# Performance work log

Measured on AMD Instinct MI355X. Metric: run time of the kernel, lower is better.

## Reference

```python
import jax, jax.numpy as jnp
import numpy as np

N, E, D, ETYPES = 20000, 200000, 256, 16

def _gelu(x):
    return jax.nn.gelu(x, approximate=False)

def setup_inputs() -> dict:
    key = jax.random.key(0)
    ks = jax.random.split(key, 24)
    s = lambda k, shape, fan: (jax.random.normal(k, shape, jnp.float32) / np.sqrt(fan)).astype(jnp.float32)
    inp = {}
    inp['node_embeddings'] = jax.random.normal(ks[0], (N, D), jnp.float32)
    inp['edge_index'] = jax.random.randint(ks[1], (2, E), 0, N, jnp.int64 if jax.config.jax_enable_x64 else jnp.int32)
    inp['edge_type'] = jax.random.randint(ks[2], (E,), 0, ETYPES, jnp.int32)
    inp['task_embedding'] = jax.random.normal(ks[3], (D,), jnp.float32)
    inp['edge_emb'] = s(ks[4], (ETYPES, D), D)
    inp['msg_W'] = s(ks[5], (D, D), D); inp['msg_b'] = jnp.zeros((D,), jnp.float32)
    inp['att_W1'] = s(ks[6], (4 * D, D), 4 * D); inp['att_b1'] = jnp.zeros((D,), jnp.float32)
    inp['att_W2'] = s(ks[7], (D, 1), D); inp['att_b2'] = jnp.zeros((1,), jnp.float32)
    inp['edge_scale'] = jnp.asarray(0.5, jnp.float32)
    inp['ma_W1'] = s(ks[8], (D, 2 * D), D); inp['ma_b1'] = jnp.zeros((2 * D,), jnp.float32)
    inp['ma_W2'] = s(ks[9], (2 * D, 2 * D), 2 * D); inp['ma_b2'] = jnp.zeros((2 * D,), jnp.float32)
    inp['up_W1'] = s(ks[10], (2 * D, D), 2 * D); inp['up_b1'] = jnp.zeros((D,), jnp.float32)
    inp['up_W2'] = s(ks[11], (D, D), D); inp['up_b2'] = jnp.zeros((D,), jnp.float32)
    inp['ua_W1'] = s(ks[12], (D, 2 * D), D); inp['ua_b1'] = jnp.zeros((2 * D,), jnp.float32)
    inp['ua_W2'] = s(ks[13], (2 * D, 2 * D), 2 * D); inp['ua_b2'] = jnp.zeros((2 * D,), jnp.float32)
    inp['ln_g'] = jnp.ones((D,), jnp.float32); inp['ln_b'] = jnp.zeros((D,), jnp.float32)
    return inp

def reference(node_embeddings, edge_index, edge_type, task_embedding, edge_emb,
              msg_W, msg_b, att_W1, att_b1, att_W2, att_b2, edge_scale,
              ma_W1, ma_b1, ma_W2, ma_b2, up_W1, up_b1, up_W2, up_b2,
              ua_W1, ua_b1, ua_W2, ua_b2, ln_g, ln_b):
    n_nodes = node_embeddings.shape[0]
    src, dst = edge_index[0], edge_index[1]
    e = edge_emb[edge_type]                       # [E, D]
    x_src = node_embeddings[src]                  # [E, D]
    x_dst = node_embeddings[dst]                  # [E, D]
    messages = (x_src + e) @ msg_W + msg_b        # [E, D]
    # edge attention over [x_src, x_dst, edge_repr, task]
    task_rep = jnp.broadcast_to(task_embedding, (src.shape[0], task_embedding.shape[0]))
    att_in = jnp.concatenate([x_src, x_dst, e, task_rep], axis=-1)  # [E, 4D]
    edge_delta = jnp.tanh(_gelu(att_in @ att_W1 + att_b1) @ att_W2 + att_b2)  # [E, 1]
    edge_weight = 1.0 + edge_scale * edge_delta   # [E, 1]
    # FiLM-style message adapter from task embedding
    ma = _gelu(task_embedding @ ma_W1 + ma_b1) @ ma_W2 + ma_b2      # [2D]
    msg_gamma, msg_beta = ma[:ma.shape[0] // 2], ma[ma.shape[0] // 2:]
    messages = messages * (1.0 + 0.5 * jnp.tanh(msg_gamma)) + msg_beta
    messages = messages * edge_weight
    # scatter-add aggregation with degree normalization
    agg = jax.ops.segment_sum(messages, dst, num_segments=n_nodes)            # [N, D]
    deg = jax.ops.segment_sum(edge_weight[:, 0], dst, num_segments=n_nodes)   # [N]
    agg = agg / jnp.maximum(deg, 1.0)[:, None]
    ua = _gelu(task_embedding @ ua_W1 + ua_b1) @ ua_W2 + ua_b2      # [2D]
    upd_gamma, upd_beta = ua[:ua.shape[0] // 2], ua[ua.shape[0] // 2:]
    agg = agg * (1.0 + 0.5 * jnp.tanh(upd_gamma)) + upd_beta
    upd_in = jnp.concatenate([node_embeddings, agg], axis=-1)       # [N, 2D]
    updated = _gelu(upd_in @ up_W1 + up_b1) @ up_W2 + up_b2         # [N, D]
    y = node_embeddings + updated
    mu = jnp.mean(y, axis=-1, keepdims=True)
    var = jnp.mean((y - mu) ** 2, axis=-1, keepdims=True)
    return (y - mu) / jnp.sqrt(var + 1e-5) * ln_g + ln_b
```

## Files before the change

kernel.cpp:

```cpp
#include <hip/hip_runtime.h>
#include <hip/hip_bf16.h>

#define NN 20000
#define NE 200000

typedef __bf16 bf16x8 __attribute__((ext_vector_type(8)));
typedef float f32x4 __attribute__((ext_vector_type(4)));
typedef unsigned short u16x8 __attribute__((ext_vector_type(8)));

constexpr int TAB_MSG_SCALE = 0;
constexpr int TAB_MSG_BETA  = 256;
constexpr int TAB_UPD_SCALE = 512;
constexpr int TAB_UPD_BETA  = 768;
constexpr int TAB_TASKC     = 1024;
constexpr int TAB_ECM       = 1280;
constexpr size_t OFF_WPRET = 40960;
constexpr size_t OFF_W1T   = 434176;
constexpr size_t OFF_W2T   = 696320;
constexpr size_t OFF_CNT   = 827392;
constexpr size_t OFF_SRCET = 907392;
constexpr size_t OFF_UPDB  = 11147392;
constexpr size_t OFF_G     = 21387392;
constexpr size_t OFF_P2B   = 41867392;
constexpr size_t WS_NEED   = 52107392;

constexpr int ROW_BLOCKS = (NN + 63)/64;
constexpr int GEMM_GRID  = ROW_BLOCKS*4;
constexpr int CSR_BLOCKS = (NE + 255)/256;

__device__ __forceinline__ float bf2f(unsigned short u){
  union { unsigned int i; float f; } v; v.i = ((unsigned int)u) << 16; return v.f;
}
__device__ __forceinline__ unsigned short f2bf(float f){
  __bf16 h = (__bf16)f; unsigned short u; __builtin_memcpy(&u, &h, 2); return u;
}
__device__ __forceinline__ float gelu_f(float x){
  return 0.5f * x * (1.0f + erff(x * 0.70710678118654752f));
}
__device__ __forceinline__ float gelu_fast(float x){
  return x / (1.0f + __expf(-1.702f * x));
}
__device__ __forceinline__ float tanh_fast(float x){
  float e = __expf(2.0f * x);
  return 1.0f - 2.0f / (e + 1.0f);
}
__device__ __forceinline__ float sum16(const float* p){
  float a = ((p[0]+p[1])+(p[2]+p[3])) + ((p[4]+p[5])+(p[6]+p[7]));
  float b = ((p[8]+p[9])+(p[10]+p[11])) + ((p[12]+p[13])+(p[14]+p[15]));
  return a + b;
}

__global__ __launch_bounds__(256) void k_setup(
    const float* __restrict__ task, const float* __restrict__ eemb,
    const float* __restrict__ msg_W, const float* __restrict__ msg_b,
    const float* __restrict__ att_W1, const float* __restrict__ att_b1,
    const float* __restrict__ ma_W1, const float* __restrict__ ma_b1,
    const float* __restrict__ ma_W2, const float* __restrict__ ma_b2,
    const float* __restrict__ ua_W1, const float* __restrict__ ua_b1,
    const float* __restrict__ ua_W2, const float* __restrict__ ua_b2,
    const float* __restrict__ up_W1, const float* __restrict__ up_W2,
    float* __restrict__ tabs,
    unsigned short* __restrict__ WpreT, unsigned short* __restrict__ W1T,
    unsigned short* __restrict__ W2T)
{
  __shared__ float s_in[512];
  __shared__ float s_h[512];
  int bb = blockIdx.x, tid = threadIdx.x;
  if (bb >= 35){
    int b = bb - 35;
    if (b < 768){
      int n = b;
      float v;
      if (n < 256)      v = msg_W[tid*256 + n];
      else if (n < 512) v = att_W1[tid*256 + (n - 256)];
      else              v = att_W1[(256 + tid)*256 + (n - 512)];
      WpreT[n*256 + tid] = f2bf(v);
    } else if (b < 1024){
      int n = b - 768;
      W1T[n*512 + tid]       = f2bf(up_W1[tid*256 + n]);
      W1T[n*512 + 256 + tid] = f2bf(up_W1[(256 + tid)*256 + n]);
    } else {
      int n = b - 1024;
      W2T[n*256 + tid] = f2bf(up_W2[tid*256 + n]);
    }
    return;
  }
  int b = bb;
  if (b < 2){
    const float* W1 = b ? ua_W1 : ma_W1;  const float* b1 = b ? ua_b1 : ma_b1;
    const float* W2 = b ? ua_W2 : ma_W2;  const float* b2 = b ? ua_b2 : ma_b2;
    s_in[tid] = task[tid];
    __syncthreads();
    #pragma unroll
    for (int jj = 0; jj < 2; ++jj){
      int j = tid + jj*256;
      float pacc[16];
      #pragma unroll
      for (int u = 0; u < 16; ++u) pacc[u] = 0.f;
      for (int k0 = 0; k0 < 256; k0 += 16){
        float wv[16];
        #pragma unroll
        for (int u = 0; u < 16; ++u) wv[u] = W1[(k0 + u)*512 + j];
        #pragma unroll
        for (int u = 0; u < 16; ++u) pacc[u] += s_in[k0 + u] * wv[u];
      }
      s_h[j] = gelu_f(b1[j] + sum16(pacc));
    }
    __syncthreads();
    float o[2];
    #pragma unroll
    for (int jj = 0; jj < 2; ++jj){
      int j = tid + jj*256;
      float pacc[16];
      #pragma unroll
      for (int u = 0; u < 16; ++u) pacc[u] = 0.f;
      for (int k0 = 0; k0 < 512; k0 += 16){
        float wv[16];
        #pragma unroll
        for (int u = 0; u < 16; ++u) wv[u] = W2[(k0 + u)*512 + j];
        #pragma unroll
        for (int u = 0; u < 16; ++u) pacc[u] += s_h[k0 + u] * wv[u];
      }
      o[jj] = b2[j] + sum16(pacc);
    }
    float* scale = tabs + (b ? TAB_UPD_SCALE : TAB_MSG_SCALE);
    float* beta  = tabs + (b ? TAB_UPD_BETA  : TAB_MSG_BETA);
    scale[tid] = 1.0f + 0.5f * tanhf(o[0]);
    beta[tid]  = o[1];
  } else if (b == 2){
    s_in[tid] = task[tid];
    __syncthreads();
    float pacc[16];
    #pragma unroll
    for (int u = 0; u < 16; ++u) pacc[u] = 0.f;
    for (int k0 = 0; k0 < 256; k0 += 16){
      float wv[16];
      #pragma unroll
      for (int u = 0; u < 16; ++u) wv[u] = att_W1[(768 + k0 + u)*256 + tid];
      #pragma unroll
      for (int u = 0; u < 16; ++u) pacc[u] += s_in[k0 + u] * wv[u];
    }
    tabs[TAB_TASKC + tid] = att_b1[tid] + sum16(pacc);
  } else if (b < 19){
    int t = b - 3;
    s_in[tid] = eemb[t*256 + tid];
    __syncthreads();
    float pacc[16];
    #pragma unroll
    for (int u = 0; u < 16; ++u) pacc[u] = 0.f;
    for (int k0 = 0; k0 < 256; k0 += 16){
      float wv[16];
      #pragma unroll
      for (int u = 0; u < 16; ++u) wv[u] = msg_W[(k0 + u)*256 + tid];
      #pragma unroll
      for (int u = 0; u < 16; ++u) pacc[u] += s_in[k0 + u] * wv[u];
    }
    tabs[TAB_ECM + t*512 + ((tid >> 2) << 3) + 4 + (tid & 3)] = msg_b[tid] + sum16(pacc);
  } else {
    int t = b - 19;
    s_in[tid] = eemb[t*256 + tid];
    __syncthreads();
    float pacc[16];
    #pragma unroll
    for (int u = 0; u < 16; ++u) pacc[u] = 0.f;
    for (int k0 = 0; k0 < 256; k0 += 16){
      float wv[16];
      #pragma unroll
      for (int u = 0; u < 16; ++u) wv[u] = att_W1[(512 + k0 + u)*256 + tid];
      #pragma unroll
      for (int u = 0; u < 16; ++u) pacc[u] += s_in[k0 + u] * wv[u];
    }
    tabs[TAB_ECM + t*512 + ((tid >> 2) << 3) + (tid & 3)] = sum16(pacc);
  }
}

__global__ __launch_bounds__(256) void k_gemm_pre(
    const float* __restrict__ X, const unsigned short* __restrict__ WpreT,
    const float* __restrict__ tabs,
    const int* __restrict__ eidx, const int* __restrict__ etype,
    unsigned short* __restrict__ G, unsigned short* __restrict__ P2b,
    int* __restrict__ cnt, unsigned int* __restrict__ srcet)
{
  __shared__ __align__(16) unsigned short s_b[16*256];
  int tid = threadIdx.x;
  int bb = blockIdx.x;
  if (bb >= GEMM_GRID){
    int e = (bb - GEMM_GRID)*256 + tid;
    if (e < NE){
      int dst = eidx[NE + e];
      int pos = atomicAdd(&cnt[dst], 1);
      srcet[((unsigned)dst << 7) + pos] =
          (unsigned int)eidx[e] | ((unsigned int)etype[e] << 16);
    }
    return;
  }
  int rb = bb >> 2, chunk = bb & 3;
  int wv = tid >> 6, lane = tid & 63;
  int m0 = rb*64 + wv*16;
  bool valid = (m0 < NN);
  int lo = lane & 15, hi = lane >> 4;
  bf16x8 a[8];
  if (valid){
    const float* xrow = X + (size_t)(m0 + lo)*256 + hi*8;
    #pragma unroll
    for (int kc = 0; kc < 8; ++kc){
      float4 f0 = *(const float4*)(xrow + kc*32);
      float4 f1 = *(const float4*)(xrow + kc*32 + 4);
      bf16x8 v;
      v[0]=(__bf16)f0.x; v[1]=(__bf16)f0.y; v[2]=(__bf16)f0.z; v[3]=(__bf16)f0.w;
      v[4]=(__bf16)f1.x; v[5]=(__bf16)f1.y; v[6]=(__bf16)f1.z; v[7]=(__bf16)f1.w;
      a[kc] = v;
    }
  }
  int sn = tid >> 4, sk0 = (tid & 15)*16;
  int sswz = (sn & 7) << 3;
  int rswz = (lo & 7) << 3;
  for (int t = 0; t < 12; ++t){
    int nt = chunk*12 + t;
    __syncthreads();
    {
      const unsigned short* gsrc = WpreT + (size_t)(nt*16 + sn)*256 + sk0;
      uint4 d0 = *(const uint4*)(gsrc);
      uint4 d1 = *(const uint4*)(gsrc + 8);
      *(uint4*)(s_b + sn*256 + (sk0 ^ sswz))       = d0;
      *(uint4*)(s_b + sn*256 + ((sk0 + 8) ^ sswz)) = d1;
    }
    __syncthreads();
    if (!valid) continue;
    f32x4 acc = {0.f, 0.f, 0.f, 0.f};
    #pragma unroll
    for (int kc = 0; kc < 8; ++kc){
      bf16x8 bfrag = *(const bf16x8*)(s_b + lo*256 + ((kc*32 + hi*8) ^ rswz));
      acc = __builtin_amdgcn_mfma_f32_16x16x32_bf16(a[kc], bfrag, acc, 0, 0, 0);
    }
    int n0 = nt*16;
    if (nt < 16){
      int j = n0 + lo;
      unsigned short* grow = G + (size_t)(m0 + hi*4)*512 + 256 + j;
      #pragma unroll
      for (int r = 0; r < 4; ++r) grow[(size_t)r*512] = f2bf(acc[r]);
    } else if (nt < 32){
      int j = n0 - 256 + lo;
      unsigned short* grow = G + (size_t)(m0 + hi*4)*512 + j;
      #pragma unroll
      for (int r = 0; r < 4; ++r) grow[(size_t)r*512] = f2bf(acc[r]);
    } else {
      int j = n0 - 512 + lo;
      float tcadd = tabs[TAB_TASKC + j];
      unsigned short* prow = P2b + (size_t)(m0 + hi*4)*256 + j;
      #pragma unroll
      for (int r = 0; r < 4; ++r) prow[(size_t)r*256] = f2bf(acc[r] + tcadd);
    }
  }
}

__global__ __launch_bounds__(256) void k_agg(
    const int* __restrict__ cnt, const unsigned int* __restrict__ srcet,
    const unsigned short* __restrict__ G, const unsigned short* __restrict__ P2b,
    const float* __restrict__ tabs, const float* __restrict__ attW2,
    const float* __restrict__ attb2, const float* __restrict__ escale,
    unsigned short* __restrict__ updB)
{
  int wv = threadIdx.x >> 6, lane = threadIdx.x & 63;
  int h = lane >> 5, l = lane & 31;
  int node = blockIdx.x*8 + wv*2 + h;
  int d0 = l*8;
  float sc = escale[0], bb = attb2[0];

  float q[8], w2v[8];
  {
    u16x8 p2 = *(const u16x8*)(P2b + (size_t)node*256 + d0);
    #pragma unroll
    for (int j = 0; j < 8; ++j) q[j] = bf2f(p2[j]);
    float4 wa = *(const float4*)(attW2 + d0);
    float4 wb = *(const float4*)(attW2 + d0 + 4);
    w2v[0]=wa.x; w2v[1]=wa.y; w2v[2]=wa.z; w2v[3]=wa.w;
    w2v[4]=wb.x; w2v[5]=wb.y; w2v[6]=wb.z; w2v[7]=wb.w;
  }
  const float* ecm_base = tabs + TAB_ECM + (l << 4);

  int start = node << 7;
  int end = start + cnt[node];
  float acc[8];
  #pragma unroll
  for (int j = 0; j < 8; ++j) acc[j] = 0.f;
  float W = 0.f;

  unsigned int se0 = 0, se1 = 0;
  u16x8 p1a = {0,0,0,0,0,0,0,0}, mma = {0,0,0,0,0,0,0,0};
  if (start < end){
    se0 = srcet[start];
    const unsigned short* gr = G + (((unsigned)(se0 & 0xFFFFu)) << 9);
    p1a = *(const u16x8*)(gr + d0);
    mma = *(const u16x8*)(gr + 256 + d0);
    if (start + 1 < end) se1 = srcet[start + 1];
  }
  for (int i = start; i < end; ++i){
    u16x8 p1b = p1a, mmb = mma;
    unsigned int se2 = 0;
    if (i + 1 < end){
      const unsigned short* gr = G + (((unsigned)(se1 & 0xFFFFu)) << 9);
      p1b = *(const u16x8*)(gr + d0);
      mmb = *(const u16x8*)(gr + 256 + d0);
    }
    if (i + 2 < end) se2 = srcet[i + 2];
    int et = (int)(se0 >> 16);
    const float* ecm = ecm_base + (et << 9);
    float4 ec0 = *(const float4*)(ecm);
    float4 em0 = *(const float4*)(ecm + 4);
    float4 ec1 = *(const float4*)(ecm + 8);
    float4 em1 = *(const float4*)(ecm + 12);
    float part =
        gelu_fast(bf2f(p1a[0]) + q[0] + ec0.x)*w2v[0]
      + gelu_fast(bf2f(p1a[1]) + q[1] + ec0.y)*w2v[1]
      + gelu_fast(bf2f(p1a[2]) + q[2] + ec0.z)*w2v[2]
      + gelu_fast(bf2f(p1a[3]) + q[3] + ec0.w)*w2v[3]
      + gelu_fast(bf2f(p1a[4]) + q[4] + ec1.x)*w2v[4]
      + gelu_fast(bf2f(p1a[5]) + q[5] + ec1.y)*w2v[5]
      + gelu_fast(bf2f(p1a[6]) + q[6] + ec1.z)*w2v[6]
      + gelu_fast(bf2f(p1a[7]) + q[7] + ec1.w)*w2v[7];
    part += __shfl_xor(part, 1);
    part += __shfl_xor(part, 2);
    part += __shfl_xor(part, 4);
    part += __shfl_xor(part, 8);
    part += __shfl_xor(part, 16);
    float w = 1.0f + sc*tanh_fast(part + bb);
    acc[0] += w*(bf2f(mma[0]) + em0.x);
    acc[1] += w*(bf2f(mma[1]) + em0.y);
    acc[2] += w*(bf2f(mma[2]) + em0.z);
    acc[3] += w*(bf2f(mma[3]) + em0.w);
    acc[4] += w*(bf2f(mma[4]) + em1.x);
    acc[5] += w*(bf2f(mma[5]) + em1.y);
    acc[6] += w*(bf2f(mma[6]) + em1.z);
    acc[7] += w*(bf2f(mma[7]) + em1.w);
    W += w;
    se0 = se1; se1 = se2; p1a = p1b; mma = mmb;
  }

  float d = fmaxf(W, 1.0f), rd = 1.0f / d;
  unsigned short st[8];
  #pragma unroll
  for (int c = 0; c < 2; ++c){
    float4 ms = *(const float4*)(tabs + TAB_MSG_SCALE + d0 + c*4);
    float4 mb = *(const float4*)(tabs + TAB_MSG_BETA  + d0 + c*4);
    float4 us = *(const float4*)(tabs + TAB_UPD_SCALE + d0 + c*4);
    float4 ub = *(const float4*)(tabs + TAB_UPD_BETA  + d0 + c*4);
    st[c*4+0] = f2bf((ms.x*acc[c*4+0] + mb.x*W)*rd*us.x + ub.x);
    st[c*4+1] = f2bf((ms.y*acc[c*4+1] + mb.y*W)*rd*us.y + ub.y);
    st[c*4+2] = f2bf((ms.z*acc[c*4+2] + mb.z*W)*rd*us.z + ub.z);
    st[c*4+3] = f2bf((ms.w*acc[c*4+3] + mb.w*W)*rd*us.w + ub.w);
  }
  *(u16x8*)(updB + (size_t)node*256 + d0) = *(u16x8*)(st);
}

__device__ __forceinline__ bf16x8 ldA(const float* xrow, const unsigned short* urow, int ke){
  if (ke < 256){
    float4 f0 = *(const float4*)(xrow + ke);
    float4 f1 = *(const float4*)(xrow + ke + 4);
    bf16x8 v;
    v[0]=(__bf16)f0.x; v[1]=(__bf16)f0.y; v[2]=(__bf16)f0.z; v[3]=(__bf16)f0.w;
    v[4]=(__bf16)f1.x; v[5]=(__bf16)f1.y; v[6]=(__bf16)f1.z; v[7]=(__bf16)f1.w;
    return v;
  }
  return *(const bf16x8*)(urow + (ke - 256));
}

__global__ __launch_bounds__(256) void k_mlp(
    const float* __restrict__ X, const unsigned short* __restrict__ updB,
    const unsigned short* __restrict__ W1T, const unsigned short* __restrict__ W2T,
    const float* __restrict__ up_b1, const float* __restrict__ up_b2,
    const float* __restrict__ ln_g, const float* __restrict__ ln_b,
    float* __restrict__ out)
{
  __shared__ __align__(16) unsigned short s_H[32*256];
  __shared__ float s_sum[4*32], s_sq[4*32];
  __shared__ float s_mu[32], s_rs[32];
  int m0 = blockIdx.x*32;
  int tid = threadIdx.x;
  int wv = tid >> 6, lane = tid & 63, lo = lane & 15, hi = lane >> 4;

  const float* x0 = X + (size_t)(m0 + lo)*256;
  const float* x1 = x0 + 16*256;
  const unsigned short* u0 = updB + (size_t)(m0 + lo)*256;
  const unsigned short* u1 = u0 + 16*256;

  f32x4 acc0[4], acc1[4];
  #pragma unroll
  for (int t = 0; t < 4; ++t){
    float b = up_b1[wv*64 + t*16 + lo];
    acc0[t] = (f32x4){b, b, b, b};
    acc1[t] = acc0[t];
  }
  #pragma unroll
  for (int kc = 0; kc < 16; ++kc){
    int ke = kc*32 + hi*8;
    bf16x8 a0 = ldA(x0, u0, ke);
    bf16x8 a1 = ldA(x1, u1, ke);
    #pragma unroll
    for (int t = 0; t < 4; ++t){
      int n = wv*64 + t*16 + lo;
      bf16x8 bf = *(const bf16x8*)(W1T + (size_t)n*512 + ke);
      acc0[t] = __builtin_amdgcn_mfma_f32_16x16x32_bf16(a0, bf, acc0[t], 0, 0, 0);
      acc1[t] = __builtin_amdgcn_mfma_f32_16x16x32_bf16(a1, bf, acc1[t], 0, 0, 0);
    }
  }
  #pragma unroll
  for (int t = 0; t < 4; ++t){
    #pragma unroll
    for (int r = 0; r < 4; ++r){
      int row0 = hi*4 + r, n = wv*64 + t*16 + lo;
      s_H[(row0 << 8) | (n ^ ((row0 & 7) << 3))] = f2bf(gelu_fast(acc0[t][r]));
      int row1 = row0 + 16;
      s_H[(row1 << 8) | (n ^ ((row1 & 7) << 3))] = f2bf(gelu_fast(acc1[t][r]));
    }
  }
  __syncthreads();

  f32x4 y0[4], y1[4];
  #pragma unroll
  for (int t = 0; t < 4; ++t){
    float b = up_b2[wv*64 + t*16 + lo];
    y0[t] = (f32x4){b, b, b, b};
    y1[t] = y0[t];
  }
  #pragma unroll
  for (int kc = 0; kc < 8; ++kc){
    int ke = kc*32 + hi*8;
    bf16x8 af0 = *(const bf16x8*)(s_H + ((lo << 8) | (ke ^ ((lo & 7) << 3))));
    int r1 = lo + 16;
    bf16x8 af1 = *(const bf16x8*)(s_H + ((r1 << 8) | (ke ^ ((r1 & 7) << 3))));
    #pragma unroll
    for (int t = 0; t < 4; ++t){
      int n = wv*64 + t*16 + lo;
      bf16x8 bf = *(const bf16x8*)(W2T + (size_t)n*256 + ke);
      y0[t] = __builtin_amdgcn_mfma_f32_16x16x32_bf16(af0, bf, y0[t], 0, 0, 0);
      y1[t] = __builtin_amdgcn_mfma_f32_16x16x32_bf16(af1, bf, y1[t], 0, 0, 0);
    }
  }

  #pragma unroll
  for (int t = 0; t < 4; ++t){
    #pragma unroll
    for (int r = 0; r < 4; ++r){
      int row0 = hi*4 + r, n = wv*64 + t*16 + lo;
      y0[t][r] += X[(size_t)(m0 + row0)*256 + n];
      y1[t][r] += X[(size_t)(m0 + row0 + 16)*256 + n];
    }
  }

  float ps[2][4], pq[2][4];
  #pragma unroll
  for (int r = 0; r < 4; ++r){
    float s0 = 0.f, q0 = 0.f, s1 = 0.f, q1 = 0.f;
    #pragma unroll
    for (int t = 0; t < 4; ++t){
      s0 += y0[t][r]; q0 += y0[t][r]*y0[t][r];
      s1 += y1[t][r]; q1 += y1[t][r]*y1[t][r];
    }
    #pragma unroll
    for (int off = 1; off < 16; off <<= 1){
      s0 += __shfl_xor(s0, off); q0 += __shfl_xor(q0, off);
      s1 += __shfl_xor(s1, off); q1 += __shfl_xor(q1, off);
    }
    ps[0][r] = s0; pq[0][r] = q0;
    ps[1][r] = s1; pq[1][r] = q1;
  }
  if (lo == 0){
    #pragma unroll
    for (int m = 0; m < 2; ++m){
      #pragma unroll
      for (int r = 0; r < 4; ++r){
        int row = m*16 + hi*4 + r;
        s_sum[wv*32 + row] = ps[m][r];
        s_sq [wv*32 + row] = pq[m][r];
      }
    }
  }
  __syncthreads();
  if (tid < 32){
    float sum = s_sum[tid] + s_sum[32 + tid] + s_sum[64 + tid] + s_sum[96 + tid];
    float sq  = s_sq[tid]  + s_sq[32 + tid]  + s_sq[64 + tid]  + s_sq[96 + tid];
    float mu = sum * (1.0f/256.0f);
    float var = sq * (1.0f/256.0f) - mu*mu;
    s_mu[tid] = mu;
    s_rs[tid] = rsqrtf(var + 1e-5f);
  }
  __syncthreads();

  #pragma unroll
  for (int t = 0; t < 4; ++t){
    int n = wv*64 + t*16 + lo;
    float lg = ln_g[n], lb = ln_b[n];
    #pragma unroll
    for (int r = 0; r < 4; ++r){
      int row0 = hi*4 + r, row1 = row0 + 16;
      out[(size_t)(m0 + row0)*256 + n] = (y0[t][r] - s_mu[row0]) * s_rs[row0] * lg + lb;
      out[(size_t)(m0 + row1)*256 + n] = (y1[t][r] - s_mu[row1]) * s_rs[row1] * lg + lb;
    }
  }
}

extern "C" void kernel_launch(void* const* d_in, const int* in_sizes, int n_in,
                              void* d_out, int out_size, void* d_ws, size_t ws_size,
                              hipStream_t stream)
{
  (void)in_sizes; (void)n_in; (void)out_size;
  if (ws_size < WS_NEED) return;
  const float* X      = (const float*)d_in[0];
  const int*   eidx   = (const int*)d_in[1];
  const int*   etype  = (const int*)d_in[2];
  const float* task   = (const float*)d_in[3];
  const float* eemb   = (const float*)d_in[4];
  const float* msg_W  = (const float*)d_in[5];
  const float* msg_b  = (const float*)d_in[6];
  const float* att_W1 = (const float*)d_in[7];
  const float* att_b1 = (const float*)d_in[8];
  const float* att_W2 = (const float*)d_in[9];
  const float* att_b2 = (const float*)d_in[10];
  const float* escale = (const float*)d_in[11];
  const float* ma_W1  = (const float*)d_in[12];
  const float* ma_b1  = (const float*)d_in[13];
  const float* ma_W2  = (const float*)d_in[14];
  const float* ma_b2  = (const float*)d_in[15];
  const float* up_W1  = (const float*)d_in[16];
  const float* up_b1  = (const float*)d_in[17];
  const float* up_W2  = (const float*)d_in[18];
  const float* up_b2  = (const float*)d_in[19];
  const float* ua_W1  = (const float*)d_in[20];
  const float* ua_b1  = (const float*)d_in[21];
  const float* ua_W2  = (const float*)d_in[22];
  const float* ua_b2  = (const float*)d_in[23];
  const float* ln_g   = (const float*)d_in[24];
  const float* ln_b   = (const float*)d_in[25];
  char* ws = (char*)d_ws;
  float* tabs = (float*)ws;
  unsigned short* WpreT = (unsigned short*)(ws + OFF_WPRET);
  unsigned short* W1T   = (unsigned short*)(ws + OFF_W1T);
  unsigned short* W2T   = (unsigned short*)(ws + OFF_W2T);
  int*          cnt   = (int*)(ws + OFF_CNT);
  unsigned int* srcet = (unsigned int*)(ws + OFF_SRCET);
  unsigned short* updB = (unsigned short*)(ws + OFF_UPDB);
  unsigned short* G    = (unsigned short*)(ws + OFF_G);
  unsigned short* P2b  = (unsigned short*)(ws + OFF_P2B);
  float* out = (float*)d_out;

  hipMemsetAsync(cnt, 0, (size_t)NN*4, stream);
  k_setup<<<1315, 256, 0, stream>>>(task, eemb, msg_W, msg_b, att_W1, att_b1,
                                    ma_W1, ma_b1, ma_W2, ma_b2,
                                    ua_W1, ua_b1, ua_W2, ua_b2,
                                    up_W1, up_W2,
                                    tabs, WpreT, W1T, W2T);
  k_gemm_pre<<<GEMM_GRID + CSR_BLOCKS, 256, 0, stream>>>(X, WpreT, tabs,
                                                         eidx, etype,
                                                         G, P2b, cnt, srcet);
  k_agg<<<NN/8, 256, 0, stream>>>(cnt, srcet, G, P2b, tabs,
                                  att_W2, att_b2, escale, updB);
  k_mlp<<<NN/32, 256, 0, stream>>>(X, updB, W1T, W2T, up_b1, up_b2,
                                   ln_g, ln_b, out);
}
```

Before: 194.6 us.

## Fuse edge aggregation into node MLP kernel via shared-memory update tile

Merges the aggregation kernel and the update MLP/LayerNorm kernel into one 512-thread kernel. Each block first aggregates 32 nodes (two passes of 16 nodes over 8 waves) into a swizzled LDS tile, then runs the two MFMA GEMMs and LayerNorm reading the aggregated half of the input from LDS. This removes the global round-trip of the bf16 update buffer and one kernel launch. In exchange the grid drops from 2500 blocks to 625, the gather phase is serialized over two nodes per wave pair, and GEMM work per wave halves, which may reduce latency hiding during the irregular gather.

```diff
diff --git a/kernel.cpp b/kernel.cpp
--- a/kernel.cpp
+++ b/kernel.cpp
@@ -19,7 +19,6 @@
 constexpr size_t OFF_W2T   = 696320;
 constexpr size_t OFF_CNT   = 827392;
 constexpr size_t OFF_SRCET = 907392;
-constexpr size_t OFF_UPDB  = 11147392;
 constexpr size_t OFF_G     = 21387392;
 constexpr size_t OFF_P2B   = 41867392;
 constexpr size_t WS_NEED   = 52107392;
@@ -254,161 +253,165 @@
   }
 }
 
-__global__ __launch_bounds__(256) void k_agg(
+__global__ __launch_bounds__(512) void k_agg_mlp(
     const int* __restrict__ cnt, const unsigned int* __restrict__ srcet,
     const unsigned short* __restrict__ G, const unsigned short* __restrict__ P2b,
     const float* __restrict__ tabs, const float* __restrict__ attW2,
     const float* __restrict__ attb2, const float* __restrict__ escale,
-    unsigned short* __restrict__ updB)
-{
-  int wv = threadIdx.x >> 6, lane = threadIdx.x & 63;
-  int h = lane >> 5, l = lane & 31;
-  int node = blockIdx.x*8 + wv*2 + h;
-  int d0 = l*8;
-  float sc = escale[0], bb = attb2[0];
-
-  float q[8], w2v[8];
-  {
-    u16x8 p2 = *(const u16x8*)(P2b + (size_t)node*256 + d0);
-    #pragma unroll
-    for (int j = 0; j < 8; ++j) q[j] = bf2f(p2[j]);
-    float4 wa = *(const float4*)(attW2 + d0);
-    float4 wb = *(const float4*)(attW2 + d0 + 4);
-    w2v[0]=wa.x; w2v[1]=wa.y; w2v[2]=wa.z; w2v[3]=wa.w;
-    w2v[4]=wb.x; w2v[5]=wb.y; w2v[6]=wb.z; w2v[7]=wb.w;
-  }
-  const float* ecm_base = tabs + TAB_ECM + (l << 4);
-
-  int start = node << 7;
-  int end = start + cnt[node];
-  float acc[8];
-  #pragma unroll
-  for (int j = 0; j < 8; ++j) acc[j] = 0.f;
-  float W = 0.f;
-
-  unsigned int se0 = 0, se1 = 0;
-  u16x8 p1a = {0,0,0,0,0,0,0,0}, mma = {0,0,0,0,0,0,0,0};
-  if (start < end){
-    se0 = srcet[start];
-    const unsigned short* gr = G + (((unsigned)(se0 & 0xFFFFu)) << 9);
-    p1a = *(const u16x8*)(gr + d0);
-    mma = *(const u16x8*)(gr + 256 + d0);
-    if (start + 1 < end) se1 = srcet[start + 1];
-  }
-  for (int i = start; i < end; ++i){
-    u16x8 p1b = p1a, mmb = mma;
-    unsigned int se2 = 0;
-    if (i + 1 < end){
-      const unsigned short* gr = G + (((unsigned)(se1 & 0xFFFFu)) << 9);
-      p1b = *(const u16x8*)(gr + d0);
-      mmb = *(const u16x8*)(gr + 256 + d0);
-    }
-    if (i + 2 < end) se2 = srcet[i + 2];
-    int et = (int)(se0 >> 16);
-    const float* ecm = ecm_base + (et << 9);
-    float4 ec0 = *(const float4*)(ecm);
-    float4 em0 = *(const float4*)(ecm + 4);
-    float4 ec1 = *(const float4*)(ecm + 8);
-    float4 em1 = *(const float4*)(ecm + 12);
-    float part =
-        gelu_fast(bf2f(p1a[0]) + q[0] + ec0.x)*w2v[0]
-      + gelu_fast(bf2f(p1a[1]) + q[1] + ec0.y)*w2v[1]
-      + gelu_fast(bf2f(p1a[2]) + q[2] + ec0.z)*w2v[2]
-      + gelu_fast(bf2f(p1a[3]) + q[3] + ec0.w)*w2v[3]
-      + gelu_fast(bf2f(p1a[4]) + q[4] + ec1.x)*w2v[4]
-      + gelu_fast(bf2f(p1a[5]) + q[5] + ec1.y)*w2v[5]
-      + gelu_fast(bf2f(p1a[6]) + q[6] + ec1.z)*w2v[6]
-      + gelu_fast(bf2f(p1a[7]) + q[7] + ec1.w)*w2v[7];
-    part += __shfl_xor(part, 1);
-    part += __shfl_xor(part, 2);
-    part += __shfl_xor(part, 4);
-    part += __shfl_xor(part, 8);
-    part += __shfl_xor(part, 16);
-    float w = 1.0f + sc*tanh_fast(part + bb);
-    acc[0] += w*(bf2f(mma[0]) + em0.x);
-    acc[1] += w*(bf2f(mma[1]) + em0.y);
-    acc[2] += w*(bf2f(mma[2]) + em0.z);
-    acc[3] += w*(bf2f(mma[3]) + em0.w);
-    acc[4] += w*(bf2f(mma[4]) + em1.x);
-    acc[5] += w*(bf2f(mma[5]) + em1.y);
-    acc[6] += w*(bf2f(mma[6]) + em1.z);
-    acc[7] += w*(bf2f(mma[7]) + em1.w);
-    W += w;
-    se0 = se1; se1 = se2; p1a = p1b; mma = mmb;
-  }
-
-  float d = fmaxf(W, 1.0f), rd = 1.0f / d;
-  unsigned short st[8];
-  #pragma unroll
-  for (int c = 0; c < 2; ++c){
-    float4 ms = *(const float4*)(tabs + TAB_MSG_SCALE + d0 + c*4);
-    float4 mb = *(const float4*)(tabs + TAB_MSG_BETA  + d0 + c*4);
-    float4 us = *(const float4*)(tabs + TAB_UPD_SCALE + d0 + c*4);
-    float4 ub = *(const float4*)(tabs + TAB_UPD_BETA  + d0 + c*4);
-    st[c*4+0] = f2bf((ms.x*acc[c*4+0] + mb.x*W)*rd*us.x + ub.x);
-    st[c*4+1] = f2bf((ms.y*acc[c*4+1] + mb.y*W)*rd*us.y + ub.y);
-    st[c*4+2] = f2bf((ms.z*acc[c*4+2] + mb.z*W)*rd*us.z + ub.z);
-    st[c*4+3] = f2bf((ms.w*acc[c*4+3] + mb.w*W)*rd*us.w + ub.w);
-  }
-  *(u16x8*)(updB + (size_t)node*256 + d0) = *(u16x8*)(st);
-}
-
-__device__ __forceinline__ bf16x8 ldA(const float* xrow, const unsigned short* urow, int ke){
-  if (ke < 256){
-    float4 f0 = *(const float4*)(xrow + ke);
-    float4 f1 = *(const float4*)(xrow + ke + 4);
-    bf16x8 v;
-    v[0]=(__bf16)f0.x; v[1]=(__bf16)f0.y; v[2]=(__bf16)f0.z; v[3]=(__bf16)f0.w;
-    v[4]=(__bf16)f1.x; v[5]=(__bf16)f1.y; v[6]=(__bf16)f1.z; v[7]=(__bf16)f1.w;
-    return v;
-  }
-  return *(const bf16x8*)(urow + (ke - 256));
-}
-
-__global__ __launch_bounds__(256) void k_mlp(
-    const float* __restrict__ X, const unsigned short* __restrict__ updB,
+    const float* __restrict__ X,
     const unsigned short* __restrict__ W1T, const unsigned short* __restrict__ W2T,
     const float* __restrict__ up_b1, const float* __restrict__ up_b2,
     const float* __restrict__ ln_g, const float* __restrict__ ln_b,
     float* __restrict__ out)
 {
+  __shared__ __align__(16) unsigned short s_upd[32*256];
   __shared__ __align__(16) unsigned short s_H[32*256];
-  __shared__ float s_sum[4*32], s_sq[4*32];
+  __shared__ float s_sum[8*32], s_sq[8*32];
   __shared__ float s_mu[32], s_rs[32];
   int m0 = blockIdx.x*32;
   int tid = threadIdx.x;
-  int wv = tid >> 6, lane = tid & 63, lo = lane & 15, hi = lane >> 4;
-
+  int wv = tid >> 6, lane = tid & 63;
+
+  {
+    int h = lane >> 5, l = lane & 31;
+    int d0 = l*8;
+    float sc = escale[0], bb = attb2[0];
+    float w2v[8];
+    {
+      float4 wa = *(const float4*)(attW2 + d0);
+      float4 wb = *(const float4*)(attW2 + d0 + 4);
+      w2v[0]=wa.x; w2v[1]=wa.y; w2v[2]=wa.z; w2v[3]=wa.w;
+      w2v[4]=wb.x; w2v[5]=wb.y; w2v[6]=wb.z; w2v[7]=wb.w;
+    }
+    const float* ecm_base = tabs + TAB_ECM + (l << 4);
+    #pragma unroll 1
+    for (int p = 0; p < 2; ++p){
+      int row = p*16 + wv*2 + h;
+      int node = m0 + row;
+      float q[8];
+      {
+        u16x8 p2 = *(const u16x8*)(P2b + (size_t)node*256 + d0);
+        #pragma unroll
+        for (int j = 0; j < 8; ++j) q[j] = bf2f(p2[j]);
+      }
+      int start = node << 7;
+      int end = start + cnt[node];
+      float acc[8];
+      #pragma unroll
+      for (int j = 0; j < 8; ++j) acc[j] = 0.f;
+      float W = 0.f;
+
+      unsigned int se0 = 0, se1 = 0;
+      u16x8 p1a = {0,0,0,0,0,0,0,0}, mma = {0,0,0,0,0,0,0,0};
+      if (start < end){
+        se0 = srcet[start];
+        const unsigned short* gr = G + (((unsigned)(se0 & 0xFFFFu)) << 9);
+        p1a = *(const u16x8*)(gr + d0);
+        mma = *(const u16x8*)(gr + 256 + d0);
+        if (start + 1 < end) se1 = srcet[start + 1];
+      }
+      for (int i = start; i < end; ++i){
+        u16x8 p1b = p1a, mmb = mma;
+        unsigned int se2 = 0;
+        if (i + 1 < end){
+          const unsigned short* gr = G + (((unsigned)(se1 & 0xFFFFu)) << 9);
+          p1b = *(const u16x8*)(gr + d0);
+          mmb = *(const u16x8*)(gr + 256 + d0);
+        }
+        if (i + 2 < end) se2 = srcet[i + 2];
+        int et = (int)(se0 >> 16);
+        const float* ecm = ecm_base + (et << 9);
+        float4 ec0 = *(const float4*)(ecm);
+        float4 em0 = *(const float4*)(ecm + 4);
+        float4 ec1 = *(const float4*)(ecm + 8);
+        float4 em1 = *(const float4*)(ecm + 12);
+        float part =
+            gelu_fast(bf2f(p1a[0]) + q[0] + ec0.x)*w2v[0]
+          + gelu_fast(bf2f(p1a[1]) + q[1] + ec0.y)*w2v[1]
+          + gelu_fast(bf2f(p1a[2]) + q[2] + ec0.z)*w2v[2]
+          + gelu_fast(bf2f(p1a[3]) + q[3] + ec0.w)*w2v[3]
+          + gelu_fast(bf2f(p1a[4]) + q[4] + ec1.x)*w2v[4]
+          + gelu_fast(bf2f(p1a[5]) + q[5] + ec1.y)*w2v[5]
+          + gelu_fast(bf2f(p1a[6]) + q[6] + ec1.z)*w2v[6]
+          + gelu_fast(bf2f(p1a[7]) + q[7] + ec1.w)*w2v[7];
+        part += __shfl_xor(part, 1);
+        part += __shfl_xor(part, 2);
+        part += __shfl_xor(part, 4);
+        part += __shfl_xor(part, 8);
+        part += __shfl_xor(part, 16);
+        float w = 1.0f + sc*tanh_fast(part + bb);
+        acc[0] += w*(bf2f(mma[0]) + em0.x);
+        acc[1] += w*(bf2f(mma[1]) + em0.y);
+        acc[2] += w*(bf2f(mma[2]) + em0.z);
+        acc[3] += w*(bf2f(mma[3]) + em0.w);
+        acc[4] += w*(bf2f(mma[4]) + em1.x);
+        acc[5] += w*(bf2f(mma[5]) + em1.y);
+        acc[6] += w*(bf2f(mma[6]) + em1.z);
+        acc[7] += w*(bf2f(mma[7]) + em1.w);
+        W += w;
+        se0 = se1; se1 = se2; p1a = p1b; mma = mmb;
+      }
+
+      float dn = fmaxf(W, 1.0f), rd = 1.0f / dn;
+      unsigned short st[8];
+      #pragma unroll
+      for (int c = 0; c < 2; ++c){
+        float4 ms = *(const float4*)(tabs + TAB_MSG_SCALE + d0 + c*4);
+        float4 mb = *(const float4*)(tabs + TAB_MSG_BETA  + d0 + c*4);
+        float4 us = *(const float4*)(tabs + TAB_UPD_SCALE + d0 + c*4);
+        float4 ub = *(const float4*)(tabs + TAB_UPD_BETA  + d0 + c*4);
+        st[c*4+0] = f2bf((ms.x*acc[c*4+0] + mb.x*W)*rd*us.x + ub.x);
+        st[c*4+1] = f2bf((ms.y*acc[c*4+1] + mb.y*W)*rd*us.y + ub.y);
+        st[c*4+2] = f2bf((ms.z*acc[c*4+2] + mb.z*W)*rd*us.z + ub.z);
+        st[c*4+3] = f2bf((ms.w*acc[c*4+3] + mb.w*W)*rd*us.w + ub.w);
+      }
+      *(u16x8*)(s_upd + row*256 + (d0 ^ ((row & 7) << 3))) = *(u16x8*)(st);
+    }
+  }
+  __syncthreads();
+
+  int lo = lane & 15, hi = lane >> 4;
   const float* x0 = X + (size_t)(m0 + lo)*256;
   const float* x1 = x0 + 16*256;
-  const unsigned short* u0 = updB + (size_t)(m0 + lo)*256;
-  const unsigned short* u1 = u0 + 16*256;
-
-  f32x4 acc0[4], acc1[4];
-  #pragma unroll
-  for (int t = 0; t < 4; ++t){
-    float b = up_b1[wv*64 + t*16 + lo];
+
+  f32x4 acc0[2], acc1[2];
+  #pragma unroll
+  for (int t = 0; t < 2; ++t){
+    float b = up_b1[wv*32 + t*16 + lo];
     acc0[t] = (f32x4){b, b, b, b};
     acc1[t] = acc0[t];
   }
   #pragma unroll
   for (int kc = 0; kc < 16; ++kc){
     int ke = kc*32 + hi*8;
-    bf16x8 a0 = ldA(x0, u0, ke);
-    bf16x8 a1 = ldA(x1, u1, ke);
-    #pragma unroll
-    for (int t = 0; t < 4; ++t){
-      int n = wv*64 + t*16 + lo;
+    bf16x8 a0, a1;
+    if (ke < 256){
+      float4 f0 = *(const float4*)(x0 + ke);
+      float4 f1 = *(const float4*)(x0 + ke + 4);
+      a0[0]=(__bf16)f0.x; a0[1]=(__bf16)f0.y; a0[2]=(__bf16)f0.z; a0[3]=(__bf16)f0.w;
+      a0[4]=(__bf16)f1.x; a0[5]=(__bf16)f1.y; a0[6]=(__bf16)f1.z; a0[7]=(__bf16)f1.w;
+      float4 g0 = *(const float4*)(x1 + ke);
+      float4 g1 = *(const float4*)(x1 + ke + 4);
+      a1[0]=(__bf16)g0.x; a1[1]=(__bf16)g0.y; a1[2]=(__bf16)g0.z; a1[3]=(__bf16)g0.w;
+      a1[4]=(__bf16)g1.x; a1[5]=(__bf16)g1.y; a1[6]=(__bf16)g1.z; a1[7]=(__bf16)g1.w;
+    } else {
+      int e = ke - 256;
+      a0 = *(const bf16x8*)(s_upd + lo*256 + (e ^ ((lo & 7) << 3)));
+      a1 = *(const bf16x8*)(s_upd + (lo + 16)*256 + (e ^ ((lo & 7) << 3)));
+    }
+    #pragma unroll
+    for (int t = 0; t < 2; ++t){
+      int n = wv*32 + t*16 + lo;
       bf16x8 bf = *(const bf16x8*)(W1T + (size_t)n*512 + ke);
       acc0[t] = __builtin_amdgcn_mfma_f32_16x16x32_bf16(a0, bf, acc0[t], 0, 0, 0);
       acc1[t] = __builtin_amdgcn_mfma_f32_16x16x32_bf16(a1, bf, acc1[t], 0, 0, 0);
     }
   }
   #pragma unroll
-  for (int t = 0; t < 4; ++t){
+  for (int t = 0; t < 2; ++t){
     #pragma unroll
     for (int r = 0; r < 4; ++r){
-      int row0 = hi*4 + r, n = wv*64 + t*16 + lo;
+      int row0 = hi*4 + r, n = wv*32 + t*16 + lo;
       s_H[(row0 << 8) | (n ^ ((row0 & 7) << 3))] = f2bf(gelu_fast(acc0[t][r]));
       int row1 = row0 + 16;
       s_H[(row1 << 8) | (n ^ ((row1 & 7) << 3))] = f2bf(gelu_fast(acc1[t][r]));
@@ -416,10 +419,10 @@
   }
   __syncthreads();
 
-  f32x4 y0[4], y1[4];
-  #pragma unroll
-  for (int t = 0; t < 4; ++t){
-    float b = up_b2[wv*64 + t*16 + lo];
+  f32x4 y0[2], y1[2];
+  #pragma unroll
+  for (int t = 0; t < 2; ++t){
+    float b = up_b2[wv*32 + t*16 + lo];
     y0[t] = (f32x4){b, b, b, b};
     y1[t] = y0[t];
   }
@@ -430,8 +433,8 @@
     int r1 = lo + 16;
     bf16x8 af1 = *(const bf16x8*)(s_H + ((r1 << 8) | (ke ^ ((r1 & 7) << 3))));
     #pragma unroll
-    for (int t = 0; t < 4; ++t){
-      int n = wv*64 + t*16 + lo;
+    for (int t = 0; t < 2; ++t){
+      int n = wv*32 + t*16 + lo;
       bf16x8 bf = *(const bf16x8*)(W2T + (size_t)n*256 + ke);
       y0[t] = __builtin_amdgcn_mfma_f32_16x16x32_bf16(af0, bf, y0[t], 0, 0, 0);
       y1[t] = __builtin_amdgcn_mfma_f32_16x16x32_bf16(af1, bf, y1[t], 0, 0, 0);
@@ -439,10 +442,10 @@
   }
 
   #pragma unroll
-  for (int t = 0; t < 4; ++t){
+  for (int t = 0; t < 2; ++t){
     #pragma unroll
     for (int r = 0; r < 4; ++r){
-      int row0 = hi*4 + r, n = wv*64 + t*16 + lo;
+      int row0 = hi*4 + r, n = wv*32 + t*16 + lo;
       y0[t][r] += X[(size_t)(m0 + row0)*256 + n];
       y1[t][r] += X[(size_t)(m0 + row0 + 16)*256 + n];
     }
@@ -453,7 +456,7 @@
   for (int r = 0; r < 4; ++r){
     float s0 = 0.f, q0 = 0.f, s1 = 0.f, q1 = 0.f;
     #pragma unroll
-    for (int t = 0; t < 4; ++t){
+    for (int t = 0; t < 2; ++t){
       s0 += y0[t][r]; q0 += y0[t][r]*y0[t][r];
       s1 += y1[t][r]; q1 += y1[t][r]*y1[t][r];
     }
@@ -478,8 +481,12 @@
   }
   __syncthreads();
   if (tid < 32){
-    float sum = s_sum[tid] + s_sum[32 + tid] + s_sum[64 + tid] + s_sum[96 + tid];
-    float sq  = s_sq[tid]  + s_sq[32 + tid]  + s_sq[64 + tid]  + s_sq[96 + tid];
+    float sum = 0.f, sq = 0.f;
+    #pragma unroll
+    for (int w8 = 0; w8 < 8; ++w8){
+      sum += s_sum[w8*32 + tid];
+      sq  += s_sq [w8*32 + tid];
+    }
     float mu = sum * (1.0f/256.0f);
     float var = sq * (1.0f/256.0f) - mu*mu;
     s_mu[tid] = mu;
@@ -488,8 +495,8 @@
   __syncthreads();
 
   #pragma unroll
-  for (int t = 0; t < 4; ++t){
-    int n = wv*64 + t*16 + lo;
+  for (int t = 0; t < 2; ++t){
+    int n = wv*32 + t*16 + lo;
     float lg = ln_g[n], lb = ln_b[n];
     #pragma unroll
     for (int r = 0; r < 4; ++r){
@@ -539,7 +546,6 @@
   unsigned short* W2T   = (unsigned short*)(ws + OFF_W2T);
   int*          cnt   = (int*)(ws + OFF_CNT);
   unsigned int* srcet = (unsigned int*)(ws + OFF_SRCET);
-  unsigned short* updB = (unsigned short*)(ws + OFF_UPDB);
   unsigned short* G    = (unsigned short*)(ws + OFF_G);
   unsigned short* P2b  = (unsigned short*)(ws + OFF_P2B);
   float* out = (float*)d_out;
@@ -553,8 +559,8 @@
   k_gemm_pre<<<GEMM_GRID + CSR_BLOCKS, 256, 0, stream>>>(X, WpreT, tabs,
                                                          eidx, etype,
                                                          G, P2b, cnt, srcet);
-  k_agg<<<NN/8, 256, 0, stream>>>(cnt, srcet, G, P2b, tabs,
-                                  att_W2, att_b2, escale, updB);
-  k_mlp<<<NN/32, 256, 0, stream>>>(X, updB, W1T, W2T, up_b1, up_b2,
-                                   ln_g, ln_b, out);
-}
+  k_agg_mlp<<<NN/32, 512, 0, stream>>>(cnt, srcet, G, P2b, tabs,
+                                       att_W2, att_b2, escale,
+                                       X, W1T, W2T, up_b1, up_b2,
+                                       ln_g, ln_b, out);
+}
```

Measured after the change: 210.2 us. 8.0% more time.
